# Optimization experiments

Measured on AMD Instinct MI355X. Metric: run time of the kernel, lower is better.

The kernel has to match this reference:

```python
import jax, jax.numpy as jnp
import numpy as np

LN_EPS = 1e-5
N_HEAD_CHANNELS = 32  # model_dim=256 -> 8 heads


def _layer_norm(x, g, b):
    m = jnp.mean(x, axis=-1, keepdims=True)
    v = jnp.mean((x - m) ** 2, axis=-1, keepdims=True)
    return (x - m) * jax.lax.rsqrt(v + LN_EPS) * g + b


def setup_inputs() -> dict:
    key = jax.random.key(0)
    ks = jax.random.split(key, 12)
    b, n, nv, f = 1, 65536, 1, 256
    s = 256  # 4 ** seq_level_attention
    w = 0.02
    d = {}
    d["x"] = jax.random.normal(ks[0], (b, n, nv, f), jnp.float32)
    d["mask"] = jnp.ones((b, n, nv), dtype=bool)
    d["pos_embeddings"] = jax.random.normal(ks[1], (nv, s, f), jnp.float32) * w
    d["W_emb"] = jax.random.normal(ks[2], (f, 2 * f), jnp.float32) * w
    d["b_emb"] = jnp.zeros((2 * f,), jnp.float32)
    d["ln1_g"] = jnp.ones((f,), jnp.float32)
    d["ln1_b"] = jnp.zeros((f,), jnp.float32)
    d["Wq"] = jax.random.normal(ks[3], (f, f), jnp.float32) * w
    d["bq"] = jnp.zeros((f,), jnp.float32)
    d["Wk"] = jax.random.normal(ks[4], (f, f), jnp.float32) * w
    d["bk"] = jnp.zeros((f,), jnp.float32)
    d["Wv"] = jax.random.normal(ks[5], (f, f), jnp.float32) * w
    d["bv"] = jnp.zeros((f,), jnp.float32)
    d["Wo"] = jax.random.normal(ks[6], (f, f), jnp.float32) * w
    d["bo"] = jnp.zeros((f,), jnp.float32)
    d["ln2_g"] = jnp.ones((f,), jnp.float32)
    d["ln2_b"] = jnp.zeros((f,), jnp.float32)
    d["W1"] = jax.random.normal(ks[7], (f, f), jnp.float32) * w
    d["W2"] = jax.random.normal(ks[8], (f, f), jnp.float32) * w
    d["gamma"] = jnp.ones((f,), jnp.float32) * 1e-6
    d["gamma_mlp"] = jnp.ones((f,), jnp.float32) * 1e-6
    return d


def reference(x, mask, pos_embeddings, W_emb, b_emb, ln1_g, ln1_b,
              Wq, bq, Wk, bk, Wv, bv, Wo, bo, ln2_g, ln2_b, W1, W2,
              gamma, gamma_mlp):
    b, n, nv, f = x.shape
    s = pos_embeddings.shape[1]          # window length = 4**seq_level
    n_seq = n // s
    n_heads = f // N_HEAD_CHANNELS
    hd = f // n_heads

    x_res = x
    # sequenize: (b, n, nv, f) -> (b, n_seq, s, nv, f)
    xs = x.reshape(b, n_seq, s, nv, f)
    ms = mask.reshape(b, n_seq, s, nv)
    # mask_update: a vertex stays valid only if its whole window is valid
    mask_update = (ms & jnp.all(ms, axis=-2, keepdims=True)).reshape(b, n, nv)

    # shift/scale from position embeddings: (nv, s, 2f) -> (s, nv, 2f)
    emb = jnp.swapaxes(pos_embeddings @ W_emb + b_emb, -2, -3)
    shift, scale = jnp.split(emb, 2, axis=-1)  # each (s, nv, f)

    xm = _layer_norm(xs, ln1_g, ln1_b) * (scale + 1.0) + shift

    B = b * n_seq
    L = s * nv
    xf = xm.reshape(B, L, f)
    mf = ms.reshape(B, L)

    def heads(t):
        return t.reshape(B, L, n_heads, hd).transpose(0, 2, 1, 3)

    q = heads(xf @ Wq + bq)
    k = heads(xf @ Wk + bk)
    v = heads(xf @ Wv + bv)

    scores = jnp.einsum('bhqd,bhkd->bhqk', q, k) / np.sqrt(hd).astype(np.float32)
    scores = scores + jnp.where(mf[:, None, None, :], 0.0, -1e9)
    attn = jax.nn.softmax(scores, axis=-1)
    out = jnp.einsum('bhqk,bhkd->bhqd', attn, v)
    out = out.transpose(0, 2, 1, 3).reshape(B, L, f) @ Wo + bo

    x = x_res + gamma * out.reshape(b, n, nv, f)
    h = _layer_norm(x, ln2_g, ln2_b) @ W1
    h = jax.nn.silu(h) @ W2
    x = x + gamma_mlp * h
    return (x, mask_update)
```

## Files before the change

### kernel.cpp

```cpp
#include <hip/hip_runtime.h>
#include <cstddef>
#include <cstdint>

typedef unsigned short u16;
typedef short s16x8 __attribute__((ext_vector_type(8)));
typedef float f32x4 __attribute__((ext_vector_type(4)));
typedef int   i32x4 __attribute__((ext_vector_type(4)));
typedef u16   u16x4 __attribute__((ext_vector_type(4)));

__device__ __forceinline__ float b2f(u16 u) {
  union { unsigned int i; float f; } v; v.i = ((unsigned int)u) << 16; return v.f;
}
__device__ __forceinline__ u16 f2b(float f) {
  union { float f; unsigned int i; } v; v.f = f;
  unsigned int r = v.i + 0x7fffu + ((v.i >> 16) & 1u);
  return (u16)(r >> 16);
}
__device__ __forceinline__ unsigned int cvt_pk(float a, float b) {
  unsigned int r;
  asm("v_cvt_pk_bf16_f32 %0, %1, %2" : "=v"(r) : "v"(a), "v"(b));
  return r;
}

__global__ __launch_bounds__(256) void transpose6(
    const float* __restrict__ w0, const float* __restrict__ w1,
    const float* __restrict__ w2, const float* __restrict__ w3,
    const float* __restrict__ w4, const float* __restrict__ w5,
    u16* __restrict__ wt)
{
  __shared__ u16 T[64][66];
  const float* src;
  switch (blockIdx.x) {
    case 0: src = w0; break; case 1: src = w1; break;
    case 2: src = w2; break; case 3: src = w3; break;
    case 4: src = w4; break; default: src = w5; break;
  }
  u16* dst = wt + (size_t)blockIdx.x * 65536;
  const int tr = (blockIdx.y & 3) * 64;
  const int tc = (blockIdx.y >> 2) * 64;
  const int lane = threadIdx.x & 63, grp = threadIdx.x >> 6;
  #pragma unroll
  for (int i = 0; i < 16; ++i) {
    const int r = grp + i * 4;
    T[lane][r] = f2b(src[(size_t)(tr + r) * 256 + tc + lane]);
  }
  __syncthreads();
  #pragma unroll
  for (int i = 0; i < 16; ++i) {
    const int j = grp + i * 4;
    dst[(size_t)(tc + j) * 256 + tr + lane] = T[j][lane];
  }
}

__global__ __launch_bounds__(256) void film_kernel(
    const float* __restrict__ pos, const float* __restrict__ Wemb,
    const float* __restrict__ bemb, float* __restrict__ shift,
    float* __restrict__ scale)
{
  __shared__ float prow[256];
  __shared__ float psum[4][64];
  const int s = blockIdx.x, t = threadIdx.x;
  const int ks = t >> 6, cl = t & 63;
  const int c = blockIdx.y * 64 + cl;
  prow[t] = pos[s * 256 + t];
  __syncthreads();
  float acc = 0.f;
  #pragma unroll 8
  for (int kk = ks * 64; kk < ks * 64 + 64; ++kk)
    acc = fmaf(prow[kk], Wemb[kk * 512 + c], acc);
  psum[ks][cl] = acc;
  __syncthreads();
  if (t < 64) {
    const int cc = blockIdx.y * 64 + t;
    const float v = psum[0][t] + psum[1][t] + psum[2][t] + psum[3][t] + bemb[cc];
    if (cc < 256) shift[s * 256 + cc] = v;
    else          scale[s * 256 + cc - 256] = v;
  }
}

__global__ __launch_bounds__(256) void ln_kernel(
    const float* __restrict__ xf,
    const float* __restrict__ shift, const float* __restrict__ scale,
    const float* __restrict__ g, const float* __restrict__ b,
    u16* __restrict__ out)
{
  const int lane = threadIdx.x & 63;
  const int l = lane & 15, grp = lane >> 4;
  const int token = blockIdx.x * 16 + (threadIdx.x >> 6) * 4 + grp;
  const size_t tb = (size_t)token * 256;
  const int spos = token & 255;

  f32x4 v[4];
  #pragma unroll
  for (int j = 0; j < 4; ++j) v[j] = *(const f32x4*)(xf + tb + 4 * l + 64 * j);
  float s = 0.f, s2 = 0.f;
  #pragma unroll
  for (int j = 0; j < 4; ++j)
    #pragma unroll
    for (int i = 0; i < 4; ++i) { s += v[j][i]; s2 += v[j][i] * v[j][i]; }
  #pragma unroll
  for (int off = 8; off >= 1; off >>= 1) {
    s  += __shfl_xor(s, off);
    s2 += __shfl_xor(s2, off);
  }
  const float mean = s * 0.00390625f;
  const float inv  = rsqrtf(s2 * 0.00390625f - mean * mean + 1e-5f);
  #pragma unroll
  for (int j = 0; j < 4; ++j) {
    const int e = 4 * l + 64 * j;
    const f32x4 gv = *(const f32x4*)(g + e);
    const f32x4 bv = *(const f32x4*)(b + e);
    const f32x4 sc = *(const f32x4*)(scale + spos * 256 + e);
    const f32x4 sh = *(const f32x4*)(shift + spos * 256 + e);
    u16x4 o;
    #pragma unroll
    for (int i = 0; i < 4; ++i) {
      float ln = (v[j][i] - mean) * inv * gv[i] + bv[i];
      ln = ln * (sc[i] + 1.0f) + sh[i];
      o[i] = f2b(ln);
    }
    *(u16x4*)(out + tb + e) = o;
  }
}

__global__ __launch_bounds__(256) void gemm_qkv(
    const u16* __restrict__ A, const u16* __restrict__ wt,
    const float* __restrict__ bq, const float* __restrict__ bk,
    const float* __restrict__ bv, u16* __restrict__ qo,
    u16* __restrict__ ko, u16* __restrict__ vo)
{
  __shared__ __align__(16) u16 Alds[128][72];
  __shared__ __align__(16) u16 Blds[128][72];
  const int bid = blockIdx.x;
  const int xcd = bid & 7, rr = bid >> 3;
  const int xx = rr % 6;
  const int yy = (rr / 6) * 8 + xcd;
  const int wsel = xx >> 1;
  const int m0 = yy * 128;
  const int n0 = (xx & 1) * 128;
  const u16* BT = wt + (size_t)wsel * 65536;
  const int t = threadIdx.x;
  const int wave = t >> 6, lane = t & 63;
  const int wm = (wave & 1) * 64, wn = (wave >> 1) * 64;
  const int lrow = lane & 15, lk = (lane >> 4) * 8;

  f32x4 acc[4][4];
  #pragma unroll
  for (int i = 0; i < 4; ++i)
    #pragma unroll
    for (int j = 0; j < 4; ++j)
      acc[i][j] = f32x4{0.f, 0.f, 0.f, 0.f};

  for (int k0 = 0; k0 < 256; k0 += 64) {
    #pragma unroll
    for (int i = 0; i < 4; ++i) {
      const int c = i * 256 + t;
      const int row = c >> 3, col = (c & 7) * 8;
      *(i32x4*)(&Alds[row][col]) = *(const i32x4*)(A  + (size_t)(m0 + row) * 256 + k0 + col);
      *(i32x4*)(&Blds[row][col]) = *(const i32x4*)(BT + (size_t)(n0 + row) * 256 + k0 + col);
    }
    __syncthreads();
    #pragma unroll
    for (int kk = 0; kk < 64; kk += 32) {
      s16x8 af[4], bf[4];
      #pragma unroll
      for (int mt = 0; mt < 4; ++mt) af[mt] = *(const s16x8*)(&Alds[wm + mt*16 + lrow][kk + lk]);
      #pragma unroll
      for (int nt = 0; nt < 4; ++nt) bf[nt] = *(const s16x8*)(&Blds[wn + nt*16 + lrow][kk + lk]);
      #pragma unroll
      for (int mt = 0; mt < 4; ++mt)
        #pragma unroll
        for (int nt = 0; nt < 4; ++nt)
          acc[mt][nt] = __builtin_amdgcn_mfma_f32_16x16x32_bf16(af[mt], bf[nt], acc[mt][nt], 0, 0, 0);
    }
    __syncthreads();
  }

  const float* bias = (wsel == 0) ? bq : (wsel == 1) ? bk : bv;
  u16* qko = (wsel == 0) ? qo : ko;
  #pragma unroll
  for (int mt = 0; mt < 4; ++mt) {
    const int mb = m0 + wm + mt*16 + (lane >> 4) * 4;
    const int w = mb >> 8, tok = mb & 255;
    #pragma unroll
    for (int nt = 0; nt < 4; ++nt) {
      const int n = n0 + wn + nt*16 + lrow;
      const int h = n >> 5, d = n & 31;
      const float bv_ = bias[n];
      if (wsel < 2) {
        #pragma unroll
        for (int r = 0; r < 4; ++r)
          qko[(size_t)w * 65536 + h * 8192 + (tok + r) * 32 + d] = f2b(acc[mt][nt][r] + bv_);
      } else {
        u16x4 pk;
        #pragma unroll
        for (int r = 0; r < 4; ++r) pk[r] = f2b(acc[mt][nt][r] + bv_);
        const int vaddr = ((tok >> 5) << 10) + (((tok >> 2) & 3) << 8)
                        + d * 8 + (((tok >> 4) & 1) << 2);
        *(u16x4*)(vo + (size_t)w * 65536 + h * 8192 + vaddr) = pk;
      }
    }
  }
}

__global__ __launch_bounds__(512) void gemm_tail(
    const u16* __restrict__ A, const u16* __restrict__ WoT,
    const u16* __restrict__ W1T, const u16* __restrict__ W2T,
    const float* __restrict__ bo, const float* __restrict__ x,
    const float* __restrict__ gam, const float* __restrict__ lg2,
    const float* __restrict__ lb2, const float* __restrict__ gml,
    float* __restrict__ outx)
{
  __shared__ __align__(16) u16 Blds[256][72];
  __shared__ __align__(16) u16 XH[64][264];
  __shared__ float LNp[4][64][2];
  __shared__ float LNm[64][2];
  const int m0 = blockIdx.x * 64;
  const int t = threadIdx.x;
  const int wave = t >> 6, lane = t & 63;
  const int wm = (wave & 1) * 32, wn = (wave >> 1) * 64;
  const int lrow = lane & 15, lk = (lane >> 4) * 8;
  const int quad = lane >> 4, col = lane & 15;

  f32x4 acc[2][4];
  #pragma unroll
  for (int i = 0; i < 2; ++i)
    #pragma unroll
    for (int j = 0; j < 4; ++j) acc[i][j] = f32x4{0.f,0.f,0.f,0.f};

  for (int p = 0; p < 4; ++p) {
    const int k0 = p * 64;
    #pragma unroll
    for (int i = 0; i < 4; ++i) {
      const int bb = i * 8192 + t * 16;
      const int n = bb >> 7, kk = (bb & 127) >> 1;
      *(i32x4*)(&Blds[n][kk]) = *(const i32x4*)(WoT + (size_t)n * 256 + k0 + kk);
    }
    __syncthreads();
    #pragma unroll
    for (int kk = 0; kk < 64; kk += 32) {
      s16x8 af[2], bf[4];
      #pragma unroll
      for (int mt = 0; mt < 2; ++mt)
        af[mt] = *(const s16x8*)(A + (size_t)(m0 + wm + mt*16 + lrow) * 256 + k0 + kk + lk);
      #pragma unroll
      for (int nt = 0; nt < 4; ++nt)
        bf[nt] = *(const s16x8*)(&Blds[wn + nt*16 + lrow][kk + lk]);
      #pragma unroll
      for (int mt = 0; mt < 2; ++mt)
        #pragma unroll
        for (int nt = 0; nt < 4; ++nt)
          acc[mt][nt] = __builtin_amdgcn_mfma_f32_16x16x32_bf16(af[mt], bf[nt], acc[mt][nt], 0, 0, 0);
    }
    __syncthreads();
  }

  unsigned int x1p[2][4][2];
  float s[2][4], s2[2][4];
  #pragma unroll
  for (int mt = 0; mt < 2; ++mt)
    #pragma unroll
    for (int r = 0; r < 4; ++r) { s[mt][r] = 0.f; s2[mt][r] = 0.f; }

  #pragma unroll
  for (int mt = 0; mt < 2; ++mt) {
    const int mb = m0 + wm + mt*16 + quad*4;
    #pragma unroll
    for (int nt = 0; nt < 4; ++nt) {
      const int n = wn + nt*16 + col;
      const float bon = bo[n], gn = gam[n];
      float v[4];
      #pragma unroll
      for (int r = 0; r < 4; ++r)
        v[r] = x[(size_t)(mb + r) * 256 + n] + gn * (acc[mt][nt][r] + bon);
      const unsigned int p0 = cvt_pk(v[0], v[1]);
      const unsigned int p1 = cvt_pk(v[2], v[3]);
      x1p[mt][nt][0] = p0;
      x1p[mt][nt][1] = p1;
      const float r0 = b2f((u16)(p0 & 0xffffu)), r1 = b2f((u16)(p0 >> 16));
      const float r2 = b2f((u16)(p1 & 0xffffu)), r3 = b2f((u16)(p1 >> 16));
      s[mt][0] += r0; s2[mt][0] += r0 * r0;
      s[mt][1] += r1; s2[mt][1] += r1 * r1;
      s[mt][2] += r2; s2[mt][2] += r2 * r2;
      s[mt][3] += r3; s2[mt][3] += r3 * r3;
    }
  }
  #pragma unroll
  for (int off = 1; off <= 8; off <<= 1) {
    #pragma unroll
    for (int mt = 0; mt < 2; ++mt)
      #pragma unroll
      for (int r = 0; r < 4; ++r) {
        s[mt][r]  += __shfl_xor(s[mt][r],  off);
        s2[mt][r] += __shfl_xor(s2[mt][r], off);
      }
  }
  if (col == 0) {
    #pragma unroll
    for (int mt = 0; mt < 2; ++mt)
      #pragma unroll
      for (int r = 0; r < 4; ++r) {
        const int row = wm + mt*16 + quad*4 + r;
        LNp[wave >> 1][row][0] = s[mt][r];
        LNp[wave >> 1][row][1] = s2[mt][r];
      }
  }
  __syncthreads();
  if (t < 64) {
    const float ss  = LNp[0][t][0] + LNp[1][t][0] + LNp[2][t][0] + LNp[3][t][0];
    const float ss2 = LNp[0][t][1] + LNp[1][t][1] + LNp[2][t][1] + LNp[3][t][1];
    const float mean = ss * 0.00390625f;
    LNm[t][0] = mean;
    LNm[t][1] = rsqrtf(ss2 * 0.00390625f - mean * mean + 1e-5f);
  }
  __syncthreads();
  #pragma unroll
  for (int mt = 0; mt < 2; ++mt) {
    #pragma unroll
    for (int nt = 0; nt < 4; ++nt) {
      const int n = wn + nt*16 + col;
      const float gg = lg2[n], bb_ = lb2[n];
      #pragma unroll
      for (int rr = 0; rr < 2; ++rr) {
        const unsigned int pk = x1p[mt][nt][rr];
        #pragma unroll
        for (int h2 = 0; h2 < 2; ++h2) {
          const int r = rr * 2 + h2;
          const int row = wm + mt*16 + quad*4 + r;
          const float rv = b2f((u16)(h2 ? (pk >> 16) : (pk & 0xffffu)));
          const float xn = (rv - LNm[row][0]) * LNm[row][1] * gg + bb_;
          XH[row][n] = f2b(xn);
        }
      }
    }
  }
  __syncthreads();

  #pragma unroll
  for (int i = 0; i < 2; ++i)
    #pragma unroll
    for (int j = 0; j < 4; ++j) acc[i][j] = f32x4{0.f,0.f,0.f,0.f};
  for (int p = 0; p < 4; ++p) {
    const int k0 = p * 64;
    #pragma unroll
    for (int i = 0; i < 4; ++i) {
      const int bb = i * 8192 + t * 16;
      const int n = bb >> 7, kk = (bb & 127) >> 1;
      *(i32x4*)(&Blds[n][kk]) = *(const i32x4*)(W1T + (size_t)n * 256 + k0 + kk);
    }
    __syncthreads();
    #pragma unroll
    for (int kk = 0; kk < 64; kk += 32) {
      s16x8 af[2], bf[4];
      #pragma unroll
      for (int mt = 0; mt < 2; ++mt)
        af[mt] = *(const s16x8*)(&XH[wm + mt*16 + lrow][k0 + kk + lk]);
      #pragma unroll
      for (int nt = 0; nt < 4; ++nt)
        bf[nt] = *(const s16x8*)(&Blds[wn + nt*16 + lrow][kk + lk]);
      #pragma unroll
      for (int mt = 0; mt < 2; ++mt)
        #pragma unroll
        for (int nt = 0; nt < 4; ++nt)
          acc[mt][nt] = __builtin_amdgcn_mfma_f32_16x16x32_bf16(af[mt], bf[nt], acc[mt][nt], 0, 0, 0);
    }
    __syncthreads();
  }
  #pragma unroll
  for (int mt = 0; mt < 2; ++mt)
    #pragma unroll
    for (int nt = 0; nt < 4; ++nt)
      #pragma unroll
      for (int r = 0; r < 4; ++r) {
        const float y = acc[mt][nt][r];
        const float hsig = __builtin_amdgcn_rcpf(1.0f + __builtin_amdgcn_exp2f(-1.442695041f * y));
        XH[wm + mt*16 + quad*4 + r][wn + nt*16 + col] = f2b(y * hsig);
        acc[mt][nt][r] = 0.0f;
      }
  __syncthreads();

  for (int p = 0; p < 4; ++p) {
    const int k0 = p * 64;
    #pragma unroll
    for (int i = 0; i < 4; ++i) {
      const int bb = i * 8192 + t * 16;
      const int n = bb >> 7, kk = (bb & 127) >> 1;
      *(i32x4*)(&Blds[n][kk]) = *(const i32x4*)(W2T + (size_t)n * 256 + k0 + kk);
    }
    __syncthreads();
    #pragma unroll
    for (int kk = 0; kk < 64; kk += 32) {
      s16x8 af[2], bf[4];
      #pragma unroll
      for (int mt = 0; mt < 2; ++mt)
        af[mt] = *(const s16x8*)(&XH[wm + mt*16 + lrow][k0 + kk + lk]);
      #pragma unroll
      for (int nt = 0; nt < 4; ++nt)
        bf[nt] = *(const s16x8*)(&Blds[wn + nt*16 + lrow][kk + lk]);
      #pragma unroll
      for (int mt = 0; mt < 2; ++mt)
        #pragma unroll
        for (int nt = 0; nt < 4; ++nt)
          acc[mt][nt] = __builtin_amdgcn_mfma_f32_16x16x32_bf16(af[mt], bf[nt], acc[mt][nt], 0, 0, 0);
    }
    __syncthreads();
  }

  #pragma unroll
  for (int mt = 0; mt < 2; ++mt) {
    const int mb = m0 + wm + mt*16 + quad*4;
    #pragma unroll
    for (int nt = 0; nt < 4; ++nt) {
      const int n = wn + nt*16 + col;
      const float gn = gml[n];
      #pragma unroll
      for (int rr = 0; rr < 2; ++rr) {
        const unsigned int pk = x1p[mt][nt][rr];
        outx[(size_t)(mb + rr*2    ) * 256 + n] = b2f((u16)(pk & 0xffffu)) + gn * acc[mt][nt][rr*2];
        outx[(size_t)(mb + rr*2 + 1) * 256 + n] = b2f((u16)(pk >> 16))     + gn * acc[mt][nt][rr*2 + 1];
      }
    }
  }
}

__global__ __launch_bounds__(512) void attn256(
    const u16* __restrict__ q, const u16* __restrict__ k,
    const u16* __restrict__ vt, const float* __restrict__ fbias,
    u16* __restrict__ out)
{
  __shared__ __align__(16) u16 KV[16384];
  __shared__ __align__(16) u16 OB[8][16][40];
  const int bid = blockIdx.x;
  const int xcd = bid & 7, rr = bid >> 3;
  const int q0 = (rr & 1) * 128;
  const int s_ = (rr >> 1) * 8 + xcd;
  const int h = s_ & 7, w = s_ >> 3;
  const int t = threadIdx.x;
  const int wave = t >> 6, lane = t & 63;
  const int col = lane & 15, quad = lane >> 4;
  const size_t hb = (size_t)w * 65536 + (size_t)h * 8192;
  const int qr0 = q0 + wave * 16;
  const float sc2 = 0.25508586f;

  {
    const char* kg = (const char*)(k + hb);
    const char* vg = (const char*)(vt + hb);
    const i32x4 r0 = *(const i32x4*)(kg + t * 16);
    const i32x4 r1 = *(const i32x4*)(kg + 8192 + t * 16);
    const i32x4 r2 = *(const i32x4*)(vg + t * 16);
    const i32x4 r3 = *(const i32x4*)(vg + 8192 + t * 16);
    char* lb = (char*)KV;
    *(i32x4*)(lb + t * 16)         = r0;
    *(i32x4*)(lb + 8192 + t * 16)  = r1;
    *(i32x4*)(lb + 16384 + t * 16) = r2;
    *(i32x4*)(lb + 24576 + t * 16) = r3;
  }

  const s16x8 af = *(const s16x8*)(q + hb + (qr0 + col) * 32 + quad * 8);
  const float* fbb = fbias + w * 256 + quad * 4;
  __syncthreads();

  f32x4 acc[16];
  #pragma unroll
  for (int tl = 0; tl < 16; ++tl) {
    const s16x8 kf = *(const s16x8*)(KV + (tl * 16 + col) * 32 + quad * 8);
    acc[tl] = __builtin_amdgcn_mfma_f32_16x16x32_bf16(kf, af, f32x4{0.f,0.f,0.f,0.f}, 0, 0, 0);
  }

  #pragma unroll
  for (int tl = 0; tl < 16; ++tl) {
    const f32x4 fb = *(const f32x4*)(fbb + tl * 16);
    #pragma unroll
    for (int r = 0; r < 4; ++r)
      acc[tl][r] = fmaf(acc[tl][r], sc2, fb[r]);
  }

  f32x4 m4 = acc[0];
  #pragma unroll
  for (int tl = 1; tl < 16; ++tl)
    #pragma unroll
    for (int r = 0; r < 4; ++r)
      m4[r] = fmaxf(m4[r], acc[tl][r]);
  float mx = fmaxf(fmaxf(m4[0], m4[1]), fmaxf(m4[2], m4[3]));
  mx = fmaxf(mx, __shfl_xor(mx, 16));
  mx = fmaxf(mx, __shfl_xor(mx, 32));

  f32x4 s4 = {0.f, 0.f, 0.f, 0.f};
  #pragma unroll
  for (int tl = 0; tl < 16; ++tl) {
    #pragma unroll
    for (int r = 0; r < 4; ++r) {
      const float e = __builtin_amdgcn_exp2f(acc[tl][r] - mx);
      acc[tl][r] = e;
      s4[r] += e;
    }
  }
  float sum = (s4[0] + s4[1]) + (s4[2] + s4[3]);
  sum += __shfl_xor(sum, 16);
  sum += __shfl_xor(sum, 32);
  const float inv = __builtin_amdgcn_rcpf(sum);

  f32x4 o0 = {0.f,0.f,0.f,0.f}, o1 = {0.f,0.f,0.f,0.f};
  const u16* vl = KV + 8192;
  #pragma unroll
  for (int s = 0; s < 8; ++s) {
    i32x4 pi;
    pi[0] = (int)cvt_pk(acc[2*s][0],     acc[2*s][1]);
    pi[1] = (int)cvt_pk(acc[2*s][2],     acc[2*s][3]);
    pi[2] = (int)cvt_pk(acc[2*s + 1][0], acc[2*s + 1][1]);
    pi[3] = (int)cvt_pk(acc[2*s + 1][2], acc[2*s + 1][3]);
    const s16x8 pf = *(const s16x8*)&pi;
    const s16x8 vf0 = *(const s16x8*)(vl + s * 1024 + quad * 256 + col * 8);
    const s16x8 vf1 = *(const s16x8*)(vl + s * 1024 + quad * 256 + col * 8 + 128);
    o0 = __builtin_amdgcn_mfma_f32_16x16x32_bf16(pf, vf0, o0, 0, 0, 0);
    o1 = __builtin_amdgcn_mfma_f32_16x16x32_bf16(pf, vf1, o1, 0, 0, 0);
  }

  f32x4 invr;
  #pragma unroll
  for (int r = 0; r < 4; ++r) invr[r] = __shfl(inv, quad * 4 + r);

  #pragma unroll
  for (int r = 0; r < 4; ++r) {
    OB[wave][quad * 4 + r][col]      = f2b(o0[r] * invr[r]);
    OB[wave][quad * 4 + r][col + 16] = f2b(o1[r] * invr[r]);
  }
  const s16x8 ov = *(const s16x8*)(&OB[wave][col][quad * 8]);
  *(s16x8*)(out + (size_t)w * 65536 + (size_t)(qr0 + col) * 256 + h * 32 + quad * 8) = ov;
}

__global__ __launch_bounds__(256) void maskup(const int* __restrict__ mask,
                                              float* __restrict__ out,
                                              float* __restrict__ fbias)
{
  __shared__ int wall[4];
  const int w = blockIdx.x, t = threadIdx.x;
  const int v = (mask[w * 256 + t] != 0) ? 1 : 0;
  const int a = __all(v);
  if ((t & 63) == 0) wall[t >> 6] = a;
  __syncthreads();
  const int allw = wall[0] & wall[1] & wall[2] & wall[3];
  out[w * 256 + t] = (v & allw) ? 1.0f : 0.0f;
  fbias[w * 256 + t] = v ? 0.0f : -1.0e9f;
}

extern "C" void kernel_launch(void* const* d_in, const int* in_sizes, int n_in,
                              void* d_out, int out_size, void* d_ws, size_t ws_size,
                              hipStream_t stream)
{
  (void)in_sizes; (void)n_in; (void)out_size; (void)ws_size;
  const float* x    = (const float*)d_in[0];
  const int*   mask = (const int*)d_in[1];
  const float* pos  = (const float*)d_in[2];
  const float* Wemb = (const float*)d_in[3];
  const float* bemb = (const float*)d_in[4];
  const float* ln1g = (const float*)d_in[5];
  const float* ln1b = (const float*)d_in[6];
  const float* Wq   = (const float*)d_in[7];
  const float* bq   = (const float*)d_in[8];
  const float* Wk   = (const float*)d_in[9];
  const float* bk   = (const float*)d_in[10];
  const float* Wv   = (const float*)d_in[11];
  const float* bv   = (const float*)d_in[12];
  const float* Wo   = (const float*)d_in[13];
  const float* bo   = (const float*)d_in[14];
  const float* ln2g = (const float*)d_in[15];
  const float* ln2b = (const float*)d_in[16];
  const float* W1   = (const float*)d_in[17];
  const float* W2   = (const float*)d_in[18];
  const float* gam  = (const float*)d_in[19];
  const float* gml  = (const float*)d_in[20];

  char* ws = (char*)d_ws;
  float* shift = (float*)ws;
  float* scale = (float*)(ws + (256 << 10));
  u16*   wt    = (u16*)(ws + (512 << 10));
  float* fbias = (float*)(ws + (1280 << 10));
  u16*   b0    = (u16*)(ws + ((size_t)2  << 20));
  u16*   b1    = (u16*)(ws + ((size_t)34 << 20));
  u16*   b2    = (u16*)(ws + ((size_t)66 << 20));
  u16*   b3    = (u16*)(ws + ((size_t)98 << 20));
  float* outx  = (float*)d_out;
  float* outm  = outx + 16777216;

  const u16* WoT = wt + 3 * 65536;
  const u16* W1T = wt + 4 * 65536;
  const u16* W2T = wt + 5 * 65536;

  transpose6<<<dim3(6, 16), 256, 0, stream>>>(Wq, Wk, Wv, Wo, W1, W2, wt);
  film_kernel<<<dim3(256, 8), 256, 0, stream>>>(pos, Wemb, bemb, shift, scale);
  maskup<<<256, 256, 0, stream>>>(mask, outm, fbias);
  ln_kernel<<<4096, 256, 0, stream>>>(x, shift, scale, ln1g, ln1b, b0);
  gemm_qkv<<<3072, 256, 0, stream>>>(b0, wt, bq, bk, bv, b1, b2, b3);
  attn256<<<4096, 512, 0, stream>>>(b1, b2, b3, fbias, b0);
  gemm_tail<<<1024, 512, 0, stream>>>(b0, WoT, W1T, W2T, bo, x, gam,
                                      ln2g, ln2b, gml, outx);
}
```

Before: 348.7 us.

## Read tail GEMM weights directly from global memory and swizzle XH in LDS

The fused output-projection/MLP tail kernel stops staging Wo, W1 and W2 tiles through a shared-memory buffer. Each wave now loads its B fragments straight from global memory (small weights that are likely L2/L1 resident), which removes the staging copies and the per-tile barriers. The XH activation buffer gets an XOR swizzle on the column index to reduce LDS bank conflicts, and an explicit barrier is added before XH is overwritten. The trade-off is redundant global loads of the weights across waves and blocks, and more exposed load latency without the LDS double-use.

```diff
diff --git a/kernel.cpp b/kernel.cpp
--- a/kernel.cpp
+++ b/kernel.cpp
@@ -211,7 +211,6 @@
     const float* __restrict__ lb2, const float* __restrict__ gml,
     float* __restrict__ outx)
 {
-  __shared__ __align__(16) u16 Blds[256][72];
   __shared__ __align__(16) u16 XH[64][264];
   __shared__ float LNp[4][64][2];
   __shared__ float LNm[64][2];
@@ -228,31 +227,20 @@
     #pragma unroll
     for (int j = 0; j < 4; ++j) acc[i][j] = f32x4{0.f,0.f,0.f,0.f};
 
-  for (int p = 0; p < 4; ++p) {
-    const int k0 = p * 64;
-    #pragma unroll
-    for (int i = 0; i < 4; ++i) {
-      const int bb = i * 8192 + t * 16;
-      const int n = bb >> 7, kk = (bb & 127) >> 1;
-      *(i32x4*)(&Blds[n][kk]) = *(const i32x4*)(WoT + (size_t)n * 256 + k0 + kk);
-    }
-    __syncthreads();
-    #pragma unroll
-    for (int kk = 0; kk < 64; kk += 32) {
-      s16x8 af[2], bf[4];
-      #pragma unroll
-      for (int mt = 0; mt < 2; ++mt)
-        af[mt] = *(const s16x8*)(A + (size_t)(m0 + wm + mt*16 + lrow) * 256 + k0 + kk + lk);
+  #pragma unroll 2
+  for (int k0 = 0; k0 < 256; k0 += 32) {
+    s16x8 af[2], bf[4];
+    #pragma unroll
+    for (int mt = 0; mt < 2; ++mt)
+      af[mt] = *(const s16x8*)(A + (size_t)(m0 + wm + mt*16 + lrow) * 256 + k0 + lk);
+    #pragma unroll
+    for (int nt = 0; nt < 4; ++nt)
+      bf[nt] = *(const s16x8*)(WoT + (size_t)(wn + nt*16 + lrow) * 256 + k0 + lk);
+    #pragma unroll
+    for (int mt = 0; mt < 2; ++mt)
       #pragma unroll
       for (int nt = 0; nt < 4; ++nt)
-        bf[nt] = *(const s16x8*)(&Blds[wn + nt*16 + lrow][kk + lk]);
-      #pragma unroll
-      for (int mt = 0; mt < 2; ++mt)
-        #pragma unroll
-        for (int nt = 0; nt < 4; ++nt)
-          acc[mt][nt] = __builtin_amdgcn_mfma_f32_16x16x32_bf16(af[mt], bf[nt], acc[mt][nt], 0, 0, 0);
-    }
-    __syncthreads();
+        acc[mt][nt] = __builtin_amdgcn_mfma_f32_16x16x32_bf16(af[mt], bf[nt], acc[mt][nt], 0, 0, 0);
   }
 
   unsigned int x1p[2][4][2];
@@ -329,7 +317,7 @@
           const int row = wm + mt*16 + quad*4 + r;
           const float rv = b2f((u16)(h2 ? (pk >> 16) : (pk & 0xffffu)));
           const float xn = (rv - LNm[row][0]) * LNm[row][1] * gg + bb_;
-          XH[row][n] = f2b(xn);
+          XH[row][n ^ ((row & 12) << 1)] = f2b(xn);
         }
       }
     }
@@ -340,32 +328,24 @@
   for (int i = 0; i < 2; ++i)
     #pragma unroll
     for (int j = 0; j < 4; ++j) acc[i][j] = f32x4{0.f,0.f,0.f,0.f};
-  for (int p = 0; p < 4; ++p) {
-    const int k0 = p * 64;
-    #pragma unroll
-    for (int i = 0; i < 4; ++i) {
-      const int bb = i * 8192 + t * 16;
-      const int n = bb >> 7, kk = (bb & 127) >> 1;
-      *(i32x4*)(&Blds[n][kk]) = *(const i32x4*)(W1T + (size_t)n * 256 + k0 + kk);
-    }
-    __syncthreads();
-    #pragma unroll
-    for (int kk = 0; kk < 64; kk += 32) {
-      s16x8 af[2], bf[4];
-      #pragma unroll
-      for (int mt = 0; mt < 2; ++mt)
-        af[mt] = *(const s16x8*)(&XH[wm + mt*16 + lrow][k0 + kk + lk]);
+  #pragma unroll 2
+  for (int k0 = 0; k0 < 256; k0 += 32) {
+    s16x8 af[2], bf[4];
+    #pragma unroll
+    for (int mt = 0; mt < 2; ++mt) {
+      const int row = wm + mt*16 + lrow;
+      af[mt] = *(const s16x8*)(&XH[row][(k0 + lk) ^ ((row & 12) << 1)]);
+    }
+    #pragma unroll
+    for (int nt = 0; nt < 4; ++nt)
+      bf[nt] = *(const s16x8*)(W1T + (size_t)(wn + nt*16 + lrow) * 256 + k0 + lk);
+    #pragma unroll
+    for (int mt = 0; mt < 2; ++mt)
       #pragma unroll
       for (int nt = 0; nt < 4; ++nt)
-        bf[nt] = *(const s16x8*)(&Blds[wn + nt*16 + lrow][kk + lk]);
-      #pragma unroll
-      for (int mt = 0; mt < 2; ++mt)
-        #pragma unroll
-        for (int nt = 0; nt < 4; ++nt)
-          acc[mt][nt] = __builtin_amdgcn_mfma_f32_16x16x32_bf16(af[mt], bf[nt], acc[mt][nt], 0, 0, 0);
-    }
-    __syncthreads();
-  }
+        acc[mt][nt] = __builtin_amdgcn_mfma_f32_16x16x32_bf16(af[mt], bf[nt], acc[mt][nt], 0, 0, 0);
+  }
+  __syncthreads();
   #pragma unroll
   for (int mt = 0; mt < 2; ++mt)
     #pragma unroll
@@ -374,36 +354,29 @@
       for (int r = 0; r < 4; ++r) {
         const float y = acc[mt][nt][r];
         const float hsig = __builtin_amdgcn_rcpf(1.0f + __builtin_amdgcn_exp2f(-1.442695041f * y));
-        XH[wm + mt*16 + quad*4 + r][wn + nt*16 + col] = f2b(y * hsig);
+        const int row = wm + mt*16 + quad*4 + r;
+        const int n = wn + nt*16 + col;
+        XH[row][n ^ ((row & 12) << 1)] = f2b(y * hsig);
         acc[mt][nt][r] = 0.0f;
       }
   __syncthreads();
 
-  for (int p = 0; p < 4; ++p) {
-    const int k0 = p * 64;
-    #pragma unroll
-    for (int i = 0; i < 4; ++i) {
-      const int bb = i * 8192 + t * 16;
-      const int n = bb >> 7, kk = (bb & 127) >> 1;
-      *(i32x4*)(&Blds[n][kk]) = *(const i32x4*)(W2T + (size_t)n * 256 + k0 + kk);
-    }
-    __syncthreads();
-    #pragma unroll
-    for (int kk = 0; kk < 64; kk += 32) {
-      s16x8 af[2], bf[4];
-      #pragma unroll
-      for (int mt = 0; mt < 2; ++mt)
-        af[mt] = *(const s16x8*)(&XH[wm + mt*16 + lrow][k0 + kk + lk]);
+  #pragma unroll 2
+  for (int k0 = 0; k0 < 256; k0 += 32) {
+    s16x8 af[2], bf[4];
+    #pragma unroll
+    for (int mt = 0; mt < 2; ++mt) {
+      const int row = wm + mt*16 + lrow;
+      af[mt] = *(const s16x8*)(&XH[row][(k0 + lk) ^ ((row & 12) << 1)]);
+    }
+    #pragma unroll
+    for (int nt = 0; nt < 4; ++nt)
+      bf[nt] = *(const s16x8*)(W2T + (size_t)(wn + nt*16 + lrow) * 256 + k0 + lk);
+    #pragma unroll
+    for (int mt = 0; mt < 2; ++mt)
       #pragma unroll
       for (int nt = 0; nt < 4; ++nt)
-        bf[nt] = *(const s16x8*)(&Blds[wn + nt*16 + lrow][kk + lk]);
-      #pragma unroll
-      for (int mt = 0; mt < 2; ++mt)
-        #pragma unroll
-        for (int nt = 0; nt < 4; ++nt)
-          acc[mt][nt] = __builtin_amdgcn_mfma_f32_16x16x32_bf16(af[mt], bf[nt], acc[mt][nt], 0, 0, 0);
-    }
-    __syncthreads();
+        acc[mt][nt] = __builtin_amdgcn_mfma_f32_16x16x32_bf16(af[mt], bf[nt], acc[mt][nt], 0, 0, 0);
   }
 
   #pragma unroll
```

New measurement: 388.9 us. 1.12x slower.
